# Performance work log

Hardware: AMD Instinct MI355X
Metric: run time of the kernel (lower is better)

## Reference

```python
import jax, jax.numpy as jnp
import numpy as np

MAX_DISP = 64  # init kwarg max_disp; feature_similarity='correlation'


def setup_inputs() -> dict:
    key = jax.random.key(0)
    k1, k2 = jax.random.split(key)
    shape = (8, 160, 320, 128)  # (b, h, w, c)
    left = jax.random.normal(k1, shape, dtype=jnp.float32)
    right = jax.random.normal(k2, shape, dtype=jnp.float32)
    return {"left_feature": left, "right_feature": right}


def reference(left_feature, right_feature):
    # Faithful to CostVolume.__call__ with feature_similarity='correlation':
    # cost[b,h,j,i] = mean_c( left[b,h,j,c] * right[b,h,j-i,c] ) for j >= i, else 0.
    b, h, w, c = left_feature.shape
    widx = jnp.arange(w)  # (w,)
    slices = []
    for i in range(MAX_DISP):  # fixed hyperparameter unroll, not a data dim
        # roll brings right[..., j-i, :] to position j along width; wrapped
        # positions j < i are masked to zero (original leaves them at init 0).
        corr = jnp.mean(left_feature * jnp.roll(right_feature, i, axis=2), axis=3)  # (b,h,w)
        corr = jnp.where(widx >= i, corr, jnp.zeros((), corr.dtype))
        slices.append(corr)
    return jnp.stack(slices, axis=-1)  # (b, h, w, max_disp)
```

## Files before the change

kernel.cpp:

```cpp
#include <hip/hip_runtime.h>

#define W 320

typedef __attribute__((ext_vector_type(8))) short   short8;
typedef __attribute__((ext_vector_type(4))) float   floatx4;

__device__ __forceinline__ unsigned int f2bf(float f) {
    unsigned int u = __float_as_uint(f);
    u += 0x7FFFu + ((u >> 16) & 1u);
    return u >> 16;
}

__global__ __launch_bounds__(640, 5)
void cost_volume_kernel(const float* __restrict__ Lg,
                        const float* __restrict__ Rg,
                        float* __restrict__ out) {
    __shared__ unsigned short S[W * 128];

    const int bh  = blockIdx.x;
    const int tid = threadIdx.x;

    const int lr    = tid >> 5;
    const int half  = tid & 1;
    const int chunk = (tid & 31) >> 1;
    const int cf    = (tid & 31) << 2;

    const float* Rrow0 = Rg + (size_t)bh * W * 128;
    #pragma unroll
    for (int p = 0; p < 16; ++p) {
        const int k = p * 20 + lr;
        floatx4 v = *(const floatx4*)(Rrow0 + (size_t)k * 128 + cf);
        uint2 d;
        d.x = f2bf(v.x) | (f2bf(v.y) << 16);
        d.y = f2bf(v.z) | (f2bf(v.w) << 16);
        const int sw = chunk ^ (k & 15);
        *(uint2*)&S[k * 128 + (sw << 3) + half * 4] = d;
    }

    __syncthreads();

    const int wave = tid >> 6;
    const int lane = tid & 63;
    const int col  = lane & 15;
    const int quad = lane >> 4;

    const float* Lrow0 = Lg + (size_t)bh * W * 128;
    float* obase = out + (size_t)bh * W * 64;

    #pragma unroll
    for (int s = 0; s < 2; ++s) {
        const int mt = wave + s * 10;
        const int m0 = mt * 16;

        const float* Arow = Lrow0 + (size_t)(m0 + col) * 128 + quad * 8;
        short8 af[4];
        #pragma unroll
        for (int ks = 0; ks < 4; ++ks) {
            floatx4 lo = *(const floatx4*)(Arow + ks * 32);
            floatx4 hi = *(const floatx4*)(Arow + ks * 32 + 4);
            short8 a;
            a[0] = (short)f2bf(lo.x); a[1] = (short)f2bf(lo.y);
            a[2] = (short)f2bf(lo.z); a[3] = (short)f2bf(lo.w);
            a[4] = (short)f2bf(hi.x); a[5] = (short)f2bf(hi.y);
            a[6] = (short)f2bf(hi.z); a[7] = (short)f2bf(hi.w);
            af[ks] = a;
        }

        floatx4 acc[5];
        #pragma unroll
        for (int t = 0; t < 5; ++t) {
            acc[t].x = 0.f; acc[t].y = 0.f; acc[t].z = 0.f; acc[t].w = 0.f;
        }

        const int kbase = m0 - 64;
        #pragma unroll
        for (int t = 0; t < 5; ++t) {
            const int kt = kbase + t * 16;
            if (kt >= 0) {
                const int krow = kt + col;
                #pragma unroll
                for (int ks = 0; ks < 4; ++ks) {
                    const int sc = (ks * 4 + quad) ^ col;
                    const short8 bf = *(const short8*)&S[krow * 128 + (sc << 3)];
                    acc[t] = __builtin_amdgcn_mfma_f32_16x16x32_bf16(af[ks], bf, acc[t], 0, 0, 0);
                }
            }
        }

        #pragma unroll
        for (int t = 0; t < 5; ++t) {
            #pragma unroll
            for (int r = 0; r < 4; ++r) {
                const int m = quad * 4 + r;
                const int i = 64 + m - t * 16 - col;
                if (i >= 0 && i < 64) {
                    obase[(size_t)(m0 + m) * 64 + i] = acc[t][r] * 0.0078125f;
                }
            }
        }
    }
}

extern "C" void kernel_launch(void* const* d_in, const int* in_sizes, int n_in,
                              void* d_out, int out_size, void* d_ws, size_t ws_size,
                              hipStream_t stream) {
    const float* L = (const float*)d_in[0];
    const float* R = (const float*)d_in[1];
    float* out = (float*)d_out;
    dim3 grid(8 * 160);
    cost_volume_kernel<<<grid, 640, 0, stream>>>(L, R, out);
}
```

Baseline: 432.0 us.

## Stream right rows through a ring buffer in LDS with software-pipelined chunks

Replaces the full 320-row LDS staging of the right feature row with a 192-row ring buffer that is filled chunk by chunk. Each iteration prefetches the next 64 right rows into registers while computing MFMA tiles for the current 64 output columns, then writes them to LDS. The block shrinks to 512 threads, with wave pairs splitting the tile work. Block indices are also remapped across batches. The aim is to cut LDS use for higher occupancy and to overlap global loads with compute. The cost is a barrier per chunk and an uneven split of work between waves.

```diff
diff --git a/kernel.cpp b/kernel.cpp
--- a/kernel.cpp
+++ b/kernel.cpp
@@ -11,13 +11,14 @@
     return u >> 16;
 }
 
-__global__ __launch_bounds__(640, 5)
+__global__ __launch_bounds__(512, 6)
 void cost_volume_kernel(const float* __restrict__ Lg,
                         const float* __restrict__ Rg,
                         float* __restrict__ out) {
-    __shared__ unsigned short S[W * 128];
+    __shared__ unsigned short S[192 * 128];
 
-    const int bh  = blockIdx.x;
+    const int lin = blockIdx.x;
+    const int bh  = (lin & 7) * 160 + (lin >> 3);
     const int tid = threadIdx.x;
 
     const int lr    = tid >> 5;
@@ -25,79 +26,115 @@
     const int chunk = (tid & 31) >> 1;
     const int cf    = (tid & 31) << 2;
 
+    const int wave = tid >> 6;
+    const int lane = tid & 63;
+    const int col  = lane & 15;
+    const int quad = lane >> 4;
+    const int lm   = wave >> 1;
+    const int g    = wave & 1;
+    const int NT   = g ? 2 : 3;
+    const int tb   = g * 3;
+
     const float* Rrow0 = Rg + (size_t)bh * W * 128;
+    const float* Lrow0 = Lg + (size_t)bh * W * 128;
+    float* obase = out + (size_t)bh * W * 64;
+
     #pragma unroll
-    for (int p = 0; p < 16; ++p) {
-        const int k = p * 20 + lr;
+    for (int p = 0; p < 4; ++p) {
+        const int k    = p * 16 + lr;
+        const int slot = k + 64;
         floatx4 v = *(const floatx4*)(Rrow0 + (size_t)k * 128 + cf);
         uint2 d;
         d.x = f2bf(v.x) | (f2bf(v.y) << 16);
         d.y = f2bf(v.z) | (f2bf(v.w) << 16);
-        const int sw = chunk ^ (k & 15);
-        *(uint2*)&S[k * 128 + (sw << 3) + half * 4] = d;
+        const int sw = chunk ^ (slot & 15);
+        *(uint2*)&S[slot * 128 + (sw << 3) + half * 4] = d;
     }
-
     __syncthreads();
 
-    const int wave = tid >> 6;
-    const int lane = tid & 63;
-    const int col  = lane & 15;
-    const int quad = lane >> 4;
-
-    const float* Lrow0 = Lg + (size_t)bh * W * 128;
-    float* obase = out + (size_t)bh * W * 64;
-
     #pragma unroll
-    for (int s = 0; s < 2; ++s) {
-        const int mt = wave + s * 10;
-        const int m0 = mt * 16;
+    for (int c = 0; c < 5; ++c) {
+        const int jc = c * 64;
+        const int m0 = jc + lm * 16;
 
         const float* Arow = Lrow0 + (size_t)(m0 + col) * 128 + quad * 8;
+        floatx4 alo[4], ahi[4];
+        #pragma unroll
+        for (int ks = 0; ks < 4; ++ks) {
+            alo[ks] = *(const floatx4*)(Arow + ks * 32);
+            ahi[ks] = *(const floatx4*)(Arow + ks * 32 + 4);
+        }
+
+        floatx4 sv[4];
+        if (c < 4) {
+            #pragma unroll
+            for (int p = 0; p < 4; ++p) {
+                const int k = jc + 64 + p * 16 + lr;
+                sv[p] = *(const floatx4*)(Rrow0 + (size_t)k * 128 + cf);
+            }
+        }
+
         short8 af[4];
         #pragma unroll
         for (int ks = 0; ks < 4; ++ks) {
-            floatx4 lo = *(const floatx4*)(Arow + ks * 32);
-            floatx4 hi = *(const floatx4*)(Arow + ks * 32 + 4);
             short8 a;
-            a[0] = (short)f2bf(lo.x); a[1] = (short)f2bf(lo.y);
-            a[2] = (short)f2bf(lo.z); a[3] = (short)f2bf(lo.w);
-            a[4] = (short)f2bf(hi.x); a[5] = (short)f2bf(hi.y);
-            a[6] = (short)f2bf(hi.z); a[7] = (short)f2bf(hi.w);
+            a[0] = (short)f2bf(alo[ks].x); a[1] = (short)f2bf(alo[ks].y);
+            a[2] = (short)f2bf(alo[ks].z); a[3] = (short)f2bf(alo[ks].w);
+            a[4] = (short)f2bf(ahi[ks].x); a[5] = (short)f2bf(ahi[ks].y);
+            a[6] = (short)f2bf(ahi[ks].z); a[7] = (short)f2bf(ahi[ks].w);
             af[ks] = a;
         }
 
-        floatx4 acc[5];
+        floatx4 acc[3];
         #pragma unroll
-        for (int t = 0; t < 5; ++t) {
+        for (int t = 0; t < 3; ++t) {
             acc[t].x = 0.f; acc[t].y = 0.f; acc[t].z = 0.f; acc[t].w = 0.f;
         }
-
-        const int kbase = m0 - 64;
         #pragma unroll
-        for (int t = 0; t < 5; ++t) {
-            const int kt = kbase + t * 16;
-            if (kt >= 0) {
-                const int krow = kt + col;
-                #pragma unroll
-                for (int ks = 0; ks < 4; ++ks) {
-                    const int sc = (ks * 4 + quad) ^ col;
-                    const short8 bf = *(const short8*)&S[krow * 128 + (sc << 3)];
-                    acc[t] = __builtin_amdgcn_mfma_f32_16x16x32_bf16(af[ks], bf, acc[t], 0, 0, 0);
+        for (int t = 0; t < 3; ++t) {
+            if (t < NT) {
+                const int kt = m0 - 64 + (tb + t) * 16;
+                if (kt >= 0) {
+                    const int x    = kt + 64 + col;
+                    const int slot = x - (x >= 192 ? 192 : 0);
+                    #pragma unroll
+                    for (int ks = 0; ks < 4; ++ks) {
+                        const int sc = (ks * 4 + quad) ^ col;
+                        const short8 bf = *(const short8*)&S[slot * 128 + (sc << 3)];
+                        acc[t] = __builtin_amdgcn_mfma_f32_16x16x32_bf16(af[ks], bf, acc[t], 0, 0, 0);
+                    }
                 }
             }
         }
 
         #pragma unroll
-        for (int t = 0; t < 5; ++t) {
-            #pragma unroll
-            for (int r = 0; r < 4; ++r) {
-                const int m = quad * 4 + r;
-                const int i = 64 + m - t * 16 - col;
-                if (i >= 0 && i < 64) {
-                    obase[(size_t)(m0 + m) * 64 + i] = acc[t][r] * 0.0078125f;
+        for (int t = 0; t < 3; ++t) {
+            if (t < NT) {
+                #pragma unroll
+                for (int r = 0; r < 4; ++r) {
+                    const int m = quad * 4 + r;
+                    const int i = 64 + m - (tb + t) * 16 - col;
+                    if (i >= 0 && i < 64) {
+                        obase[(size_t)(m0 + m) * 64 + i] = acc[t][r] * 0.0078125f;
+                    }
                 }
             }
         }
+
+        if (c < 4) {
+            #pragma unroll
+            for (int p = 0; p < 4; ++p) {
+                const int x    = jc + 128 + p * 16 + lr;
+                const int slot = x - (x >= 192 ? 192 : 0);
+                uint2 d;
+                d.x = f2bf(sv[p].x) | (f2bf(sv[p].y) << 16);
+                d.y = f2bf(sv[p].z) | (f2bf(sv[p].w) << 16);
+                const int sw = chunk ^ (slot & 15);
+                *(uint2*)&S[slot * 128 + (sw << 3) + half * 4] = d;
+            }
+        }
+
+        __syncthreads();
     }
 }
 
@@ -108,5 +145,5 @@
     const float* R = (const float*)d_in[1];
     float* out = (float*)d_out;
     dim3 grid(8 * 160);
-    cost_volume_kernel<<<grid, 640, 0, stream>>>(L, R, out);
+    cost_volume_kernel<<<grid, 512, 0, stream>>>(L, R, out);
 }
```

Measured after the change: 470.7 us. 1.09x slower.

## Replace LDS staging with per-wave register sliding window over right tiles

Applied to the files above, without the earlier changes.

Drops the shared-memory bf16 copy of the right row and the block barrier. Each of four waves now owns five consecutive 16-column tiles and keeps a rotating window of five converted right-feature fragments in registers, software-pipelining the global loads of the next left and right tiles behind the MFMA work. Block size goes from 640 to 256 threads and block indices are remapped to interleave batches. This trades LDS traffic and synchronisation for heavy register use, which may lower occupancy, and each wave also reloads overlapping right tiles from global memory.

```diff
diff --git a/kernel.cpp b/kernel.cpp
--- a/kernel.cpp
+++ b/kernel.cpp
@@ -11,93 +11,98 @@
     return u >> 16;
 }
 
-__global__ __launch_bounds__(640, 5)
+#define LOAD8(buf, base, toff) do {                                         \
+    const float* p_ = (base) + (size_t)(toff) * 2048;                       \
+    _Pragma("unroll")                                                       \
+    for (int q_ = 0; q_ < 4; ++q_) {                                        \
+        buf[2*q_]   = *(const floatx4*)(p_ + q_*32);                        \
+        buf[2*q_+1] = *(const floatx4*)(p_ + q_*32 + 4);                    \
+    } } while (0)
+
+#define CONV8(dst, buf) do {                                                \
+    _Pragma("unroll")                                                       \
+    for (int q_ = 0; q_ < 4; ++q_) {                                        \
+        short8 x_;                                                          \
+        x_[0] = (short)f2bf(buf[2*q_].x);   x_[1] = (short)f2bf(buf[2*q_].y);   \
+        x_[2] = (short)f2bf(buf[2*q_].z);   x_[3] = (short)f2bf(buf[2*q_].w);   \
+        x_[4] = (short)f2bf(buf[2*q_+1].x); x_[5] = (short)f2bf(buf[2*q_+1].y); \
+        x_[6] = (short)f2bf(buf[2*q_+1].z); x_[7] = (short)f2bf(buf[2*q_+1].w); \
+        (dst)[q_] = x_;                                                     \
+    } } while (0)
+
+__global__ __launch_bounds__(256, 2)
 void cost_volume_kernel(const float* __restrict__ Lg,
                         const float* __restrict__ Rg,
                         float* __restrict__ out) {
-    __shared__ unsigned short S[W * 128];
-
-    const int bh  = blockIdx.x;
+    const int lin = blockIdx.x;
+    const int bh  = (lin & 7) * 160 + (lin >> 3);
     const int tid = threadIdx.x;
-
-    const int lr    = tid >> 5;
-    const int half  = tid & 1;
-    const int chunk = (tid & 31) >> 1;
-    const int cf    = (tid & 31) << 2;
-
-    const float* Rrow0 = Rg + (size_t)bh * W * 128;
-    #pragma unroll
-    for (int p = 0; p < 16; ++p) {
-        const int k = p * 20 + lr;
-        floatx4 v = *(const floatx4*)(Rrow0 + (size_t)k * 128 + cf);
-        uint2 d;
-        d.x = f2bf(v.x) | (f2bf(v.y) << 16);
-        d.y = f2bf(v.z) | (f2bf(v.w) << 16);
-        const int sw = chunk ^ (k & 15);
-        *(uint2*)&S[k * 128 + (sw << 3) + half * 4] = d;
-    }
-
-    __syncthreads();
-
-    const int wave = tid >> 6;
+    const int w    = tid >> 6;
     const int lane = tid & 63;
     const int col  = lane & 15;
     const int quad = lane >> 4;
 
-    const float* Lrow0 = Lg + (size_t)bh * W * 128;
+    const float* Rb = Rg + ((size_t)bh * W + col) * 128 + quad * 8;
+    const float* Lb = Lg + ((size_t)bh * W + col) * 128 + quad * 8;
     float* obase = out + (size_t)bh * W * 64;
 
+    floatx4 rbufA[8], rbufB[8], abuf[8];
+    short8  Bf[5][4];
+    short8  Af[4];
+
+    const int T0 = 5 * w;
+
+    if (T0 >= 4) LOAD8(rbufA, Rb, T0 - 4);
+    if (T0 >= 3) LOAD8(rbufB, Rb, T0 - 3);
+    LOAD8(abuf, Lb, T0);
+    if (T0 >= 4) CONV8(Bf[1], rbufA);
+    if (T0 >= 2) LOAD8(rbufA, Rb, T0 - 2);
+    if (T0 >= 3) CONV8(Bf[2], rbufB);
+    if (T0 >= 1) LOAD8(rbufB, Rb, T0 - 1);
+    if (T0 >= 2) CONV8(Bf[3], rbufA);
+    LOAD8(rbufA, Rb, T0);
+    if (T0 >= 1) CONV8(Bf[4], rbufB);
+    CONV8(Bf[0], rbufA);
+
     #pragma unroll
-    for (int s = 0; s < 2; ++s) {
-        const int mt = wave + s * 10;
-        const int m0 = mt * 16;
+    for (int u = 0; u < 5; ++u) {
+        CONV8(Af, abuf);
 
-        const float* Arow = Lrow0 + (size_t)(m0 + col) * 128 + quad * 8;
-        short8 af[4];
-        #pragma unroll
-        for (int ks = 0; ks < 4; ++ks) {
-            floatx4 lo = *(const floatx4*)(Arow + ks * 32);
-            floatx4 hi = *(const floatx4*)(Arow + ks * 32 + 4);
-            short8 a;
-            a[0] = (short)f2bf(lo.x); a[1] = (short)f2bf(lo.y);
-            a[2] = (short)f2bf(lo.z); a[3] = (short)f2bf(lo.w);
-            a[4] = (short)f2bf(hi.x); a[5] = (short)f2bf(hi.y);
-            a[6] = (short)f2bf(hi.z); a[7] = (short)f2bf(hi.w);
-            af[ks] = a;
+        if (u < 4) {
+            LOAD8(abuf,  Lb, T0 + u + 1);
+            LOAD8(rbufA, Rb, T0 + u + 1);
         }
 
         floatx4 acc[5];
         #pragma unroll
-        for (int t = 0; t < 5; ++t) {
-            acc[t].x = 0.f; acc[t].y = 0.f; acc[t].z = 0.f; acc[t].w = 0.f;
+        for (int v = 0; v < 5; ++v) {
+            acc[v].x = 0.f; acc[v].y = 0.f; acc[v].z = 0.f; acc[v].w = 0.f;
         }
 
-        const int kbase = m0 - 64;
         #pragma unroll
-        for (int t = 0; t < 5; ++t) {
-            const int kt = kbase + t * 16;
-            if (kt >= 0) {
-                const int krow = kt + col;
+        for (int v = 0; v < 5; ++v) {
+            if (T0 + u + v >= 4) {
                 #pragma unroll
                 for (int ks = 0; ks < 4; ++ks) {
-                    const int sc = (ks * 4 + quad) ^ col;
-                    const short8 bf = *(const short8*)&S[krow * 128 + (sc << 3)];
-                    acc[t] = __builtin_amdgcn_mfma_f32_16x16x32_bf16(af[ks], bf, acc[t], 0, 0, 0);
+                    acc[v] = __builtin_amdgcn_mfma_f32_16x16x32_bf16(
+                        Af[ks], Bf[(u + 1 + v) % 5][ks], acc[v], 0, 0, 0);
                 }
             }
         }
 
+        float* orow = obase + (size_t)(T0 + u) * 16 * 64;
         #pragma unroll
-        for (int t = 0; t < 5; ++t) {
+        for (int v = 0; v < 5; ++v) {
             #pragma unroll
             for (int r = 0; r < 4; ++r) {
                 const int m = quad * 4 + r;
-                const int i = 64 + m - t * 16 - col;
-                if (i >= 0 && i < 64) {
-                    obase[(size_t)(m0 + m) * 64 + i] = acc[t][r] * 0.0078125f;
-                }
+                const int i = 64 - 16 * v + m - col;
+                const bool ok = (v == 0) ? (m < col) : (v == 4) ? (m >= col) : true;
+                if (ok) orow[(size_t)m * 64 + i] = acc[v][r] * 0.0078125f;
             }
         }
+
+        if (u < 4) CONV8(Bf[(u + 1) % 5], rbufA);
     }
 }
 
@@ -108,5 +113,5 @@
     const float* R = (const float*)d_in[1];
     float* out = (float*)d_out;
     dim3 grid(8 * 160);
-    cost_volume_kernel<<<grid, 640, 0, stream>>>(L, R, out);
+    cost_volume_kernel<<<grid, 256, 0, stream>>>(L, R, out);
 }
```

New measurement: 443.1 us. 2.6% more time.
